# Kernel tuning notes

Measured on AMD Instinct MI355X. Metric: run time of the kernel, lower is better.

Reference implementation:

```python
import jax, jax.numpy as jnp
import numpy as np

B, S, E = 2, 1024, 2048
NH = 8          # num attention heads
KVH = 1         # num key/value heads (GQA)
DH = E // NH    # head dim = 256
CAP = 15.0      # gate soft cap
EPS = 1e-6


def setup_inputs() -> dict:
    key = jax.random.key(0)
    ks = jax.random.split(key, 11)
    g = lambda k, shape, sc=0.02: (jax.random.normal(k, shape, jnp.float32) * sc)
    return {
        "x": jax.random.normal(ks[0], (B, S, E), jnp.float32),
        "Wq": g(ks[1], (E, NH * DH)),
        "Wk": g(ks[2], (E, KVH * DH)),
        "Wv": g(ks[3], (E, KVH * DH)),
        "Wog": g(ks[4], (E, E)),
        "Wi": g(ks[5], (E, NH)),
        "bi": g(ks[6], (NH,), 0.1),
        "Wf": g(ks[7], (E, NH)),
        "bf": jnp.ones((NH,), jnp.float32) * 2.0,  # bias forget gate open, as in xLSTM practice
        "gamma": jnp.ones((E,), jnp.float32),       # multihead layernorm weight
        "Wout": g(ks[8], (E, E)),
    }


def _soft_cap(z):
    return CAP * jnp.tanh(z / CAP)


def _repeat_kv(h, n_rep):
    # (B, KVH, S, DH) -> (B, KVH*n_rep, S, DH)
    if n_rep == 1:
        return h
    b, kvh, s, d = h.shape
    return jnp.broadcast_to(h[:, :, None], (b, kvh, n_rep, s, d)).reshape(b, kvh * n_rep, s, d)


def reference(x, Wq, Wk, Wv, Wog, Wi, bi, Wf, bf, gamma, Wout):
    # --- projections ---
    q = (x @ Wq).reshape(B, S, NH, DH).transpose(0, 2, 1, 3)          # (B,NH,S,DH)
    k = (x @ Wk).reshape(B, S, KVH, DH).transpose(0, 2, 1, 3)         # (B,KVH,S,DH)
    v = (x @ Wv).reshape(B, S, KVH, DH).transpose(0, 2, 1, 3)
    k = _repeat_kv(k, NH // KVH)
    v = _repeat_kv(v, NH // KVH)
    o_preact = x @ Wog                                                # (B,S,E)
    i_pre = _soft_cap(x @ Wi + bi).transpose(0, 2, 1)                 # (B,NH,S)
    f_pre = _soft_cap(x @ Wf + bf).transpose(0, 2, 1)                 # (B,NH,S)

    # --- parallel (stabilized) mLSTM backend ---
    logf = jax.nn.log_sigmoid(f_pre)
    cf = jnp.cumsum(logf, axis=-1)                                    # (B,NH,S)
    mat_logf = cf[:, :, :, None] - cf[:, :, None, :]                  # (B,NH,S,S)
    ltr = jnp.tril(jnp.ones((S, S), dtype=bool))
    mat_logD = jnp.where(ltr, mat_logf, -jnp.inf) + i_pre[:, :, None, :]
    vecM = jnp.max(mat_logD, axis=-1, keepdims=True)                  # (B,NH,S,1)
    matD = jnp.exp(mat_logD - vecM)
    matS = jnp.einsum('bhsd,bhtd->bhst', q, k) * (DH ** -0.5)
    matCt = matS * matD
    vecN = jnp.maximum(jnp.abs(matCt.sum(-1, keepdims=True)), jnp.exp(-vecM))
    matC = matCt / (vecN + EPS)
    h = jnp.einsum('bhst,bhtd->bhsd', matC, v)                        # (B,NH,S,DH)

    # --- multihead layernorm (per-head, float32 reductions) ---
    h = h.transpose(0, 2, 1, 3)                                       # (B,S,NH,DH)
    hf = h.astype(jnp.float32)
    mu = hf.mean(-1, keepdims=True)
    var = hf.var(-1, keepdims=True)
    h_norm = ((hf - mu) * jax.lax.rsqrt(var + EPS)).astype(h.dtype)
    h_norm = (h_norm * gamma.reshape(NH, DH)).reshape(B, S, E)

    # --- output gate + projection ---
    y = (jax.nn.sigmoid(o_preact) * h_norm) @ Wout
    return y
```

## Files before the change

### kernel.cpp

```cpp
#include <hip/hip_runtime.h>
#include <math.h>

#define S_LEN  1024
#define EMB    2048
#define NH_    8
#define DH_    256
#define TOKENS 2048
#define NBH    16
#define NQKVO  4608

typedef __attribute__((ext_vector_type(4))) float    f32x4;
typedef __attribute__((ext_vector_type(8))) _Float16 f16x8;
typedef __attribute__((ext_vector_type(4))) _Float16 f16x4;

__device__ __forceinline__ _Float16 f2h(float f) { return (_Float16)f; }

__device__ __forceinline__ void gload16(const void* g, void* l) {
  __builtin_amdgcn_global_load_lds(
      (const __attribute__((address_space(1))) void*)g,
      (__attribute__((address_space(3))) void*)l, 16, 0, 0);
}

__global__ __launch_bounds__(256) void transpose_all_kernel(
    const float* __restrict__ Wq, const float* __restrict__ Wk,
    const float* __restrict__ Wv, const float* __restrict__ Wog,
    const float* __restrict__ Wout,
    _Float16* __restrict__ WcatT, _Float16* __restrict__ WoutT)
{
  int t = blockIdx.x;
  const float* in; _Float16* out; int ldi, ct;
  if (t < 1024)      { in = Wq;   out = WcatT;                    ldi = 2048; ct = 32; }
  else if (t < 1152) { t -= 1024; in = Wk;  out = WcatT + (long)2048 * EMB; ldi = 256; ct = 4; }
  else if (t < 1280) { t -= 1152; in = Wv;  out = WcatT + (long)2304 * EMB; ldi = 256; ct = 4; }
  else if (t < 2304) { t -= 1280; in = Wog; out = WcatT + (long)2560 * EMB; ldi = 2048; ct = 32; }
  else               { t -= 2304; in = Wout; out = WoutT;         ldi = 2048; ct = 32; }
  const long c0 = (long)(t % ct) * 64, r0 = (long)(t / ct) * 64;
  __shared__ float tl[64][65];
  const int lx = threadIdx.x & 63, ly = threadIdx.x >> 6;
  #pragma unroll
  for (int i = 0; i < 16; ++i)
    tl[ly + i * 4][lx] = in[(r0 + ly + i * 4) * ldi + c0 + lx];
  __syncthreads();
  #pragma unroll
  for (int i = 0; i < 16; ++i)
    out[(c0 + ly + i * 4) * EMB + r0 + lx] = f2h(tl[lx][ly + i * 4]);
}

template<typename TIN>
__global__ __launch_bounds__(256) void transpose_cast_kernel(
    const TIN* __restrict__ in, long ldi, _Float16* __restrict__ out, long ldo,
    long sIn, long sOut)
{
  __shared__ float t[64][65];
  const int lx = threadIdx.x & 63, ly = threadIdx.x >> 6;
  const long r0 = (long)blockIdx.y * 64, c0 = (long)blockIdx.x * 64;
  const TIN* ip = in + (long)blockIdx.z * sIn;
  _Float16* op = out + (long)blockIdx.z * sOut;
  #pragma unroll
  for (int i = 0; i < 16; ++i)
    t[ly + i * 4][lx] = (float)ip[(r0 + ly + i * 4) * ldi + c0 + lx];
  __syncthreads();
  #pragma unroll
  for (int i = 0; i < 16; ++i)
    op[(c0 + ly + i * 4) * ldo + r0 + lx] = f2h(t[lx][ly + i * 4]);
}

template<typename CT, int BM>
__global__ __launch_bounds__(256) void gemm_bt_kernel(
    const _Float16* __restrict__ Ag, const _Float16* __restrict__ Btg,
    CT* __restrict__ Cg, int K, int lda, int ldb, int ldc,
    long sA, long sB, long sC, int zdivB, int mtiles, int causal)
{
  constexpr int MR = BM / 32;
  __shared__ _Float16 As[3][BM * 32];
  __shared__ _Float16 Bs[3][128 * 32];
  const int tid = threadIdx.x;
  const int lane = tid & 63, wid = tid >> 6;
  const int cpx = gridDim.x >> 3;
  const int wg = ((int)blockIdx.x & 7) * cpx + ((int)blockIdx.x >> 3);
  const int m0 = (wg % mtiles) * BM;
  const int n0 = (wg / mtiles) * 128;
  const int z  = blockIdx.z;
  const _Float16* Ap = Ag + (long)z * sA + (long)m0 * lda;
  const _Float16* Bp = Btg + (long)(z / zdivB) * sB + (long)n0 * ldb;
  const int wr = wid >> 1, wc = wid & 1;
  const int lrow = lane & 15, kseg = lane >> 4;
  const int kl = causal ? ((m0 + BM < K) ? m0 + BM : K) : K;

  auto stage = [&](int b, int k0) {
    #pragma unroll
    for (int i = 0; i < BM / 64; ++i) {
      const int cbase = (i * 4 + wid) * 64;
      const int row = (cbase >> 2) + (lane >> 2);
      const int src = ((lane & 3) ^ ((row >> 1) & 3)) * 8;
      gload16(Ap + (long)row * lda + k0 + src, (char*)As[b] + cbase * 16);
    }
    #pragma unroll
    for (int i = 0; i < 2; ++i) {
      const int cbase = (i * 4 + wid) * 64;
      const int row = (cbase >> 2) + (lane >> 2);
      const int src = ((lane & 3) ^ ((row >> 1) & 3)) * 8;
      gload16(Bp + (long)row * ldb + k0 + src, (char*)Bs[b] + cbase * 16);
    }
  };

  const int nt = kl >> 5;
  f32x4 acc[MR][4] = {};
  stage(0, 0);
  if (nt > 1) stage(1, 32);
  for (int t = 0; t < nt; ++t) {
    if (t + 2 < nt) {
      stage((t + 2) % 3, (t + 2) * 32);
      asm volatile("s_waitcnt vmcnt(8)" ::: "memory");
    } else if (t + 1 < nt) {
      asm volatile("s_waitcnt vmcnt(4)" ::: "memory");
    } else {
      asm volatile("s_waitcnt vmcnt(0)" ::: "memory");
    }
    __builtin_amdgcn_s_barrier();
    __builtin_amdgcn_sched_barrier(0);
    const int buf = t % 3;
    f16x8 fa[MR], fb[4];
    #pragma unroll
    for (int m = 0; m < MR; ++m) {
      const int row = wr * (BM / 2) + m * 16 + lrow;
      fa[m] = *(const f16x8*)&As[buf][row * 32 + ((kseg ^ ((row >> 1) & 3)) << 3)];
    }
    #pragma unroll
    for (int n = 0; n < 4; ++n) {
      const int row = wc * 64 + n * 16 + lrow;
      fb[n] = *(const f16x8*)&Bs[buf][row * 32 + ((kseg ^ ((row >> 1) & 3)) << 3)];
    }
    #pragma unroll
    for (int m = 0; m < MR; ++m)
      #pragma unroll
      for (int n = 0; n < 4; ++n)
        acc[m][n] = __builtin_amdgcn_mfma_f32_16x16x32_f16(fa[m], fb[n], acc[m][n], 0, 0, 0);
    __builtin_amdgcn_s_barrier();
  }
  CT* Cp = Cg + (long)z * sC;
  #pragma unroll
  for (int m = 0; m < MR; ++m)
    #pragma unroll
    for (int n = 0; n < 4; ++n)
      #pragma unroll
      for (int i = 0; i < 4; ++i) {
        const int r = m0 + wr * (BM / 2) + m * 16 + kseg * 4 + i;
        const int c = n0 + wc * 64 + n * 16 + lrow;
        Cp[(long)r * ldc + c] = (CT)acc[m][n][i];
      }
}

__global__ __launch_bounds__(256) void proj_if_cast_kernel(
    const float* __restrict__ x, const float* __restrict__ Wi, const float* __restrict__ bi,
    const float* __restrict__ Wf, const float* __restrict__ bfg,
    _Float16* __restrict__ xh, float* __restrict__ ip, float* __restrict__ fp)
{
  const int tok = blockIdx.x;
  const int tid = threadIdx.x;
  const float* xr = x + (long)tok * EMB;
  float ai[8] = {}, af[8] = {};
  #pragma unroll
  for (int j = 0; j < 8; ++j) {
    const int e = tid + j * 256;
    const float xe = xr[e];
    xh[(long)tok * EMB + e] = f2h(xe);
    const float4* wi4 = (const float4*)(Wi + (long)e * 8);
    const float4* wf4 = (const float4*)(Wf + (long)e * 8);
    const float4 a0 = wi4[0], a1 = wi4[1], b0 = wf4[0], b1 = wf4[1];
    ai[0] += xe * a0.x; ai[1] += xe * a0.y; ai[2] += xe * a0.z; ai[3] += xe * a0.w;
    ai[4] += xe * a1.x; ai[5] += xe * a1.y; ai[6] += xe * a1.z; ai[7] += xe * a1.w;
    af[0] += xe * b0.x; af[1] += xe * b0.y; af[2] += xe * b0.z; af[3] += xe * b0.w;
    af[4] += xe * b1.x; af[5] += xe * b1.y; af[6] += xe * b1.z; af[7] += xe * b1.w;
  }
  #pragma unroll
  for (int hh = 0; hh < 8; ++hh)
    for (int off = 32; off; off >>= 1) {
      ai[hh] += __shfl_xor(ai[hh], off);
      af[hh] += __shfl_xor(af[hh], off);
    }
  __shared__ float red[4][16];
  const int lane = tid & 63, wid = tid >> 6;
  if (lane == 0) {
    #pragma unroll
    for (int hh = 0; hh < 8; ++hh) { red[wid][hh] = ai[hh]; red[wid][hh + 8] = af[hh]; }
  }
  __syncthreads();
  if (tid < 16) {
    const float v = red[0][tid] + red[1][tid] + red[2][tid] + red[3][tid];
    const int b = tok >> 10, s = tok & 1023;
    if (tid < 8) {
      const float zv = v + bi[tid];
      ip[(long)(b * NH_ + tid) * S_LEN + s] = 15.0f * tanhf(zv * (1.0f / 15.0f));
    } else {
      const int hh = tid - 8;
      const float zv = v + bfg[hh];
      fp[(long)(b * NH_ + hh) * S_LEN + s] = 15.0f * tanhf(zv * (1.0f / 15.0f));
    }
  }
}

__global__ __launch_bounds__(1024) void gates_kernel(
    const float* __restrict__ fp, const float* __restrict__ ip,
    float* __restrict__ aArr, float* __restrict__ mArr, float* __restrict__ vMArr)
{
  const int bh = blockIdx.x;
  const int s = threadIdx.x;
  __shared__ float sh[1024];
  const float f = fp[(long)bh * S_LEN + s];
  const float lsg = fminf(f, 0.0f) - log1pf(expf(-fabsf(f)));
  float v = lsg;
  sh[s] = v; __syncthreads();
  for (int off = 1; off < 1024; off <<= 1) {
    const float o = (s >= off) ? sh[s - off] : 0.0f;
    __syncthreads();
    v += o; sh[s] = v;
    __syncthreads();
  }
  const float cf = v;
  const float a = ip[(long)bh * S_LEN + s] - cf;
  v = a;
  sh[s] = v; __syncthreads();
  for (int off = 1; off < 1024; off <<= 1) {
    const float o = (s >= off) ? sh[s - off] : -3.0e38f;
    __syncthreads();
    v = fmaxf(v, o); sh[s] = v;
    __syncthreads();
  }
  aArr[(long)bh * S_LEN + s] = a;
  mArr[(long)bh * S_LEN + s] = v;
  vMArr[(long)bh * S_LEN + s] = cf + v;
}

__global__ __launch_bounds__(256) void att_fused_kernel(
    const _Float16* __restrict__ qkvo, const _Float16* __restrict__ vt,
    const float* __restrict__ aArr, const float* __restrict__ mArr,
    const float* __restrict__ vMArr, _Float16* __restrict__ hb)
{
  __shared__ _Float16 Qs[2][32 * 256];
  __shared__ _Float16 Ws[2][32 * 128];
  __shared__ float nsh[2][4][32];
  __shared__ float invs[2][32];
  const int tid = threadIdx.x;
  const int lane = tid & 63, wid = tid >> 6;
  const int bh = blockIdx.y;
  const int b = bh >> 3, h = bh & 7;
  const int r0[2] = { (int)blockIdx.x * 32, (31 - (int)blockIdx.x) * 32 };
  const _Float16* Qg = qkvo + (long)(b * S_LEN) * NQKVO + h * DH_;
  const _Float16* Kg = qkvo + (long)(b * S_LEN) * NQKVO + 2048;
  const _Float16* Vt = vt + (long)b * DH_ * S_LEN;
  const float* aA = aArr + (long)bh * S_LEN;
  const float* mA = mArr + (long)bh * S_LEN;
  const int lrow = lane & 15, kseg = lane >> 4;
  const int tbase = 32 * wid;

  #pragma unroll
  for (int i = 0; i < 8; ++i) {
    const int cbase = (i * 4 + wid) * 64;
    const int c = cbase + lane;
    const int sub = c >> 10, row = (c >> 5) & 31, slot = c & 31;
    gload16(Qg + (long)(r0[sub] + row) * NQKVO + (slot ^ (row & 7)) * 8,
            (char*)Qs + cbase * 16);
  }

  float m_s[2][2][4];
  #pragma unroll
  for (int sub = 0; sub < 2; ++sub)
    #pragma unroll
    for (int m = 0; m < 2; ++m)
      #pragma unroll
      for (int i = 0; i < 4; ++i)
        m_s[sub][m][i] = mA[r0[sub] + m * 16 + kseg * 4 + i];
  __syncthreads();

  f32x4 hacc[2][2][4] = {};
  float nacc[2][2][4] = {};
  for (int n0 = 0; n0 <= r0[1]; n0 += 128) {
    f32x4 acc[2][2][2] = {};
    f16x8 fb[2], fbn[2];
    #pragma unroll
    for (int n = 0; n < 2; ++n)
      fb[n] = *(const f16x8*)(Kg + (long)(n0 + tbase + n * 16 + lrow) * NQKVO + kseg * 8);
    #pragma unroll
    for (int k0 = 0; k0 < DH_; k0 += 32) {
      if (k0 + 32 < DH_) {
        #pragma unroll
        for (int n = 0; n < 2; ++n)
          fbn[n] = *(const f16x8*)(Kg + (long)(n0 + tbase + n * 16 + lrow) * NQKVO + k0 + 32 + kseg * 8);
      }
      const int chunk = (k0 >> 3) + kseg;
      __builtin_amdgcn_s_setprio(1);
      #pragma unroll
      for (int sub = 0; sub < 2; ++sub) {
        if (n0 > r0[sub]) continue;
        #pragma unroll
        for (int m = 0; m < 2; ++m) {
          const int qrow = m * 16 + lrow;
          const f16x8 fa = *(const f16x8*)&Qs[sub][qrow * 256 + ((chunk ^ (qrow & 7)) << 3)];
          #pragma unroll
          for (int n = 0; n < 2; ++n)
            acc[sub][m][n] = __builtin_amdgcn_mfma_f32_16x16x32_f16(fa, fb[n], acc[sub][m][n], 0, 0, 0);
        }
      }
      __builtin_amdgcn_s_setprio(0);
      fb[0] = fbn[0]; fb[1] = fbn[1];
    }
    float a_t[2];
    #pragma unroll
    for (int n = 0; n < 2; ++n) a_t[n] = aA[n0 + tbase + n * 16 + lrow];
    #pragma unroll
    for (int sub = 0; sub < 2; ++sub) {
      if (n0 > r0[sub]) continue;
      #pragma unroll
      for (int m = 0; m < 2; ++m)
        #pragma unroll
        for (int n = 0; n < 2; ++n)
          #pragma unroll
          for (int i = 0; i < 4; ++i) {
            const int sr = m * 16 + kseg * 4 + i;
            const int t  = tbase + n * 16 + lrow;
            float w = 0.0f;
            if (n0 + t <= r0[sub] + sr)
              w = acc[sub][m][n][i] * 0.0625f * expf(a_t[n] - m_s[sub][m][i]);
            nacc[sub][m][i] += w;
            Ws[sub][sr * 128 + (((t >> 3) ^ ((sr & 7) << 1)) << 3) + (t & 7)] = f2h(w);
          }
    }
    f16x8 vb[4], vbn[4];
    #pragma unroll
    for (int n = 0; n < 4; ++n)
      vb[n] = *(const f16x8*)(Vt + (long)(64 * wid + n * 16 + lrow) * S_LEN + n0 + kseg * 8);
    __syncthreads();
    #pragma unroll
    for (int kt = 0; kt < 128; kt += 32) {
      if (kt + 32 < 128) {
        #pragma unroll
        for (int n = 0; n < 4; ++n)
          vbn[n] = *(const f16x8*)(Vt + (long)(64 * wid + n * 16 + lrow) * S_LEN + n0 + kt + 32 + kseg * 8);
      }
      const int chunk = (kt >> 3) + kseg;
      __builtin_amdgcn_s_setprio(1);
      #pragma unroll
      for (int sub = 0; sub < 2; ++sub) {
        if (n0 > r0[sub]) continue;
        #pragma unroll
        for (int m = 0; m < 2; ++m) {
          const int row = m * 16 + lrow;
          const f16x8 wa = *(const f16x8*)&Ws[sub][row * 128 + ((chunk ^ ((row & 7) << 1)) << 3)];
          #pragma unroll
          for (int n = 0; n < 4; ++n)
            hacc[sub][m][n] = __builtin_amdgcn_mfma_f32_16x16x32_f16(wa, vb[n], hacc[sub][m][n], 0, 0, 0);
        }
      }
      __builtin_amdgcn_s_setprio(0);
      #pragma unroll
      for (int n = 0; n < 4; ++n) vb[n] = vbn[n];
    }
    __syncthreads();
  }
  #pragma unroll
  for (int sub = 0; sub < 2; ++sub)
    #pragma unroll
    for (int m = 0; m < 2; ++m)
      #pragma unroll
      for (int i = 0; i < 4; ++i) {
        float v = nacc[sub][m][i];
        v += __shfl_xor(v, 1); v += __shfl_xor(v, 2);
        v += __shfl_xor(v, 4); v += __shfl_xor(v, 8);
        if (lrow == 0) nsh[sub][wid][m * 16 + kseg * 4 + i] = v;
      }
  __syncthreads();
  if (tid < 64) {
    const int sub = tid >> 5, sr = tid & 31;
    const float tot = nsh[sub][0][sr] + nsh[sub][1][sr] + nsh[sub][2][sr] + nsh[sub][3][sr];
    const float vm = vMArr[(long)bh * S_LEN + r0[sub] + sr];
    const float vecN = fmaxf(fabsf(tot), expf(-vm));
    invs[sub][sr] = 1.0f / (vecN + 1e-6f);
  }
  __syncthreads();
  #pragma unroll
  for (int sub = 0; sub < 2; ++sub)
    #pragma unroll
    for (int m = 0; m < 2; ++m)
      #pragma unroll
      for (int n = 0; n < 4; ++n)
        #pragma unroll
        for (int i = 0; i < 4; ++i) {
          const int row = m * 16 + kseg * 4 + i;
          const int d = 64 * wid + n * 16 + lrow;
          hb[((long)bh * S_LEN + r0[sub] + row) * DH_ + d] = f2h(hacc[sub][m][n][i] * invs[sub][row]);
        }
}

__global__ __launch_bounds__(256) void ln_gate_kernel(
    const _Float16* __restrict__ hbuf,
    const _Float16* __restrict__ qkvo, const float* __restrict__ gamma,
    _Float16* __restrict__ u)
{
  const int wid = threadIdx.x >> 6, lane = threadIdx.x & 63;
  const int row = blockIdx.x * 4 + wid;
  const int tok = row >> 3, h = row & 7;
  const int b = tok >> 10, s = tok & 1023;
  const int bh = b * NH_ + h;
  const f16x4 hv = *(const f16x4*)(hbuf + ((long)bh * S_LEN + s) * DH_ + lane * 4);
  const float v0 = (float)hv[0], v1 = (float)hv[1], v2 = (float)hv[2], v3 = (float)hv[3];
  float s1 = v0 + v1 + v2 + v3;
  float s2 = v0 * v0 + v1 * v1 + v2 * v2 + v3 * v3;
  for (int off = 32; off; off >>= 1) { s1 += __shfl_xor(s1, off); s2 += __shfl_xor(s2, off); }
  const float mu = s1 * (1.0f / 256.0f);
  const float var = s2 * (1.0f / 256.0f) - mu * mu;
  const float rs = rsqrtf(var + 1e-6f);
  const float4 g = *(const float4*)(gamma + h * DH_ + lane * 4);
  const f16x4 ov = *(const f16x4*)(qkvo + (long)tok * NQKVO + 2560 + h * DH_ + lane * 4);
  f16x4 res;
  res[0] = f2h((v0 - mu) * rs * g.x * (1.0f / (1.0f + expf(-(float)ov[0]))));
  res[1] = f2h((v1 - mu) * rs * g.y * (1.0f / (1.0f + expf(-(float)ov[1]))));
  res[2] = f2h((v2 - mu) * rs * g.z * (1.0f / (1.0f + expf(-(float)ov[2]))));
  res[3] = f2h((v3 - mu) * rs * g.w * (1.0f / (1.0f + expf(-(float)ov[3]))));
  *(f16x4*)(u + (long)tok * EMB + h * DH_ + lane * 4) = res;
}

extern "C" void kernel_launch(void* const* d_in, const int* in_sizes, int n_in,
                              void* d_out, int out_size, void* d_ws, size_t ws_size,
                              hipStream_t stream)
{
  (void)in_sizes; (void)n_in; (void)out_size; (void)ws_size;
  const float* x     = (const float*)d_in[0];
  const float* Wq    = (const float*)d_in[1];
  const float* Wk    = (const float*)d_in[2];
  const float* Wv    = (const float*)d_in[3];
  const float* Wog   = (const float*)d_in[4];
  const float* Wi    = (const float*)d_in[5];
  const float* bi    = (const float*)d_in[6];
  const float* Wf    = (const float*)d_in[7];
  const float* bfg   = (const float*)d_in[8];
  const float* gamma = (const float*)d_in[9];
  const float* Wout  = (const float*)d_in[10];

  char* base = (char*)d_ws;
  size_t off = 0;
  auto take = [&](size_t bytes) -> char* {
    char* p = base + off;
    off += (bytes + 255) & ~(size_t)255;
    return p;
  };
  _Float16* xh    = (_Float16*)take((size_t)TOKENS * EMB * 2);
  _Float16* WcatT = (_Float16*)take((size_t)NQKVO * EMB * 2);
  _Float16* WoutT = (_Float16*)take((size_t)EMB * EMB * 2);
  _Float16* qkvo  = (_Float16*)take((size_t)TOKENS * NQKVO * 2);
  _Float16* vt    = (_Float16*)take((size_t)2 * DH_ * S_LEN * 2);
  _Float16* hb    = (_Float16*)take((size_t)NBH * S_LEN * DH_ * 2);
  float*    ip    = (float*)take((size_t)NBH * S_LEN * 4);
  float*    fp    = (float*)take((size_t)NBH * S_LEN * 4);
  float*    aA    = (float*)take((size_t)NBH * S_LEN * 4);
  float*    mA    = (float*)take((size_t)NBH * S_LEN * 4);
  float*    vM    = (float*)take((size_t)NBH * S_LEN * 4);
  _Float16* ub    = xh;
  float*    y     = (float*)d_out;

  const dim3 blk(256);
  proj_if_cast_kernel<<<dim3(TOKENS), blk, 0, stream>>>(x, Wi, bi, Wf, bfg, xh, ip, fp);
  transpose_all_kernel<<<dim3(3328), blk, 0, stream>>>(Wq, Wk, Wv, Wog, Wout, WcatT, WoutT);
  gemm_bt_kernel<_Float16, 128><<<dim3(36 * 16), blk, 0, stream>>>(
      xh, WcatT, qkvo, EMB, EMB, EMB, NQKVO, 0L, 0L, 0L, 1, 16, 0);
  transpose_cast_kernel<_Float16><<<dim3(4, 16, 2), blk, 0, stream>>>(
      qkvo + 2304, NQKVO, vt, S_LEN, (long)S_LEN * NQKVO, (long)DH_ * S_LEN);
  gates_kernel<<<dim3(NBH), dim3(1024), 0, stream>>>(fp, ip, aA, mA, vM);
  att_fused_kernel<<<dim3(16, NBH), blk, 0, stream>>>(qkvo, vt, aA, mA, vM, hb);
  ln_gate_kernel<<<dim3(TOKENS * NH_ / 4), blk, 0, stream>>>(hb, qkvo, gamma, ub);
  gemm_bt_kernel<float, 128><<<dim3(16 * 16), blk, 0, stream>>>(
      ub, WoutT, y, EMB, EMB, EMB, EMB, 0L, 0L, 0L, 1, 16, 0);
}
```

Measured before the change: 191.5 us.

## Double attention block to eight waves, splitting key and head-dim work per wave

The fused attention kernel now runs 512 threads (8 waves) per block instead of 256. Each wave handles 16 key columns instead of 32 in the QK^T stage and 32 head-dim columns instead of 64 in the PV stage, and the normalizer reduction now sums over 8 waves. The grid is only 256 blocks, so the aim is more waves in flight to hide latency and lower per-wave register pressure. The cost is more barrier participants and less MFMA work per wave between syncs.

```diff
diff --git a/kernel.cpp b/kernel.cpp
--- a/kernel.cpp
+++ b/kernel.cpp
@@ -232,14 +232,14 @@
   vMArr[(long)bh * S_LEN + s] = cf + v;
 }
 
-__global__ __launch_bounds__(256) void att_fused_kernel(
+__global__ __launch_bounds__(512) void att_fused_kernel(
     const _Float16* __restrict__ qkvo, const _Float16* __restrict__ vt,
     const float* __restrict__ aArr, const float* __restrict__ mArr,
     const float* __restrict__ vMArr, _Float16* __restrict__ hb)
 {
   __shared__ _Float16 Qs[2][32 * 256];
   __shared__ _Float16 Ws[2][32 * 128];
-  __shared__ float nsh[2][4][32];
+  __shared__ float nsh[2][8][32];
   __shared__ float invs[2][32];
   const int tid = threadIdx.x;
   const int lane = tid & 63, wid = tid >> 6;
@@ -252,11 +252,12 @@
   const float* aA = aArr + (long)bh * S_LEN;
   const float* mA = mArr + (long)bh * S_LEN;
   const int lrow = lane & 15, kseg = lane >> 4;
-  const int tbase = 32 * wid;
-
-  #pragma unroll
-  for (int i = 0; i < 8; ++i) {
-    const int cbase = (i * 4 + wid) * 64;
+  const int tbase = 16 * wid;
+  const int dbase = 32 * wid;
+
+  #pragma unroll
+  for (int i = 0; i < 4; ++i) {
+    const int cbase = (i * 8 + wid) * 64;
     const int c = cbase + lane;
     const int sub = c >> 10, row = (c >> 5) & 31, slot = c & 31;
     gload16(Qg + (long)(r0[sub] + row) * NQKVO + (slot ^ (row & 7)) * 8,
@@ -273,21 +274,16 @@
         m_s[sub][m][i] = mA[r0[sub] + m * 16 + kseg * 4 + i];
   __syncthreads();
 
-  f32x4 hacc[2][2][4] = {};
+  f32x4 hacc[2][2][2] = {};
   float nacc[2][2][4] = {};
   for (int n0 = 0; n0 <= r0[1]; n0 += 128) {
-    f32x4 acc[2][2][2] = {};
-    f16x8 fb[2], fbn[2];
-    #pragma unroll
-    for (int n = 0; n < 2; ++n)
-      fb[n] = *(const f16x8*)(Kg + (long)(n0 + tbase + n * 16 + lrow) * NQKVO + kseg * 8);
+    f32x4 acc[2][2] = {};
+    f16x8 fb, fbn;
+    fb = *(const f16x8*)(Kg + (long)(n0 + tbase + lrow) * NQKVO + kseg * 8);
     #pragma unroll
     for (int k0 = 0; k0 < DH_; k0 += 32) {
-      if (k0 + 32 < DH_) {
-        #pragma unroll
-        for (int n = 0; n < 2; ++n)
-          fbn[n] = *(const f16x8*)(Kg + (long)(n0 + tbase + n * 16 + lrow) * NQKVO + k0 + 32 + kseg * 8);
-      }
+      if (k0 + 32 < DH_)
+        fbn = *(const f16x8*)(Kg + (long)(n0 + tbase + lrow) * NQKVO + k0 + 32 + kseg * 8);
       const int chunk = (k0 >> 3) + kseg;
       __builtin_amdgcn_s_setprio(1);
       #pragma unroll
@@ -297,46 +293,40 @@
         for (int m = 0; m < 2; ++m) {
           const int qrow = m * 16 + lrow;
           const f16x8 fa = *(const f16x8*)&Qs[sub][qrow * 256 + ((chunk ^ (qrow & 7)) << 3)];
-          #pragma unroll
-          for (int n = 0; n < 2; ++n)
-            acc[sub][m][n] = __builtin_amdgcn_mfma_f32_16x16x32_f16(fa, fb[n], acc[sub][m][n], 0, 0, 0);
+          acc[sub][m] = __builtin_amdgcn_mfma_f32_16x16x32_f16(fa, fb, acc[sub][m], 0, 0, 0);
         }
       }
       __builtin_amdgcn_s_setprio(0);
-      fb[0] = fbn[0]; fb[1] = fbn[1];
-    }
-    float a_t[2];
-    #pragma unroll
-    for (int n = 0; n < 2; ++n) a_t[n] = aA[n0 + tbase + n * 16 + lrow];
+      fb = fbn;
+    }
+    const float a_t = aA[n0 + tbase + lrow];
     #pragma unroll
     for (int sub = 0; sub < 2; ++sub) {
       if (n0 > r0[sub]) continue;
       #pragma unroll
       for (int m = 0; m < 2; ++m)
         #pragma unroll
-        for (int n = 0; n < 2; ++n)
-          #pragma unroll
-          for (int i = 0; i < 4; ++i) {
-            const int sr = m * 16 + kseg * 4 + i;
-            const int t  = tbase + n * 16 + lrow;
-            float w = 0.0f;
-            if (n0 + t <= r0[sub] + sr)
-              w = acc[sub][m][n][i] * 0.0625f * expf(a_t[n] - m_s[sub][m][i]);
-            nacc[sub][m][i] += w;
-            Ws[sub][sr * 128 + (((t >> 3) ^ ((sr & 7) << 1)) << 3) + (t & 7)] = f2h(w);
-          }
-    }
-    f16x8 vb[4], vbn[4];
-    #pragma unroll
-    for (int n = 0; n < 4; ++n)
-      vb[n] = *(const f16x8*)(Vt + (long)(64 * wid + n * 16 + lrow) * S_LEN + n0 + kseg * 8);
+        for (int i = 0; i < 4; ++i) {
+          const int sr = m * 16 + kseg * 4 + i;
+          const int t  = tbase + lrow;
+          float w = 0.0f;
+          if (n0 + t <= r0[sub] + sr)
+            w = acc[sub][m][i] * 0.0625f * expf(a_t - m_s[sub][m][i]);
+          nacc[sub][m][i] += w;
+          Ws[sub][sr * 128 + (((t >> 3) ^ ((sr & 7) << 1)) << 3) + (t & 7)] = f2h(w);
+        }
+    }
+    f16x8 vb[2], vbn[2];
+    #pragma unroll
+    for (int n = 0; n < 2; ++n)
+      vb[n] = *(const f16x8*)(Vt + (long)(dbase + n * 16 + lrow) * S_LEN + n0 + kseg * 8);
     __syncthreads();
     #pragma unroll
     for (int kt = 0; kt < 128; kt += 32) {
       if (kt + 32 < 128) {
         #pragma unroll
-        for (int n = 0; n < 4; ++n)
-          vbn[n] = *(const f16x8*)(Vt + (long)(64 * wid + n * 16 + lrow) * S_LEN + n0 + kt + 32 + kseg * 8);
+        for (int n = 0; n < 2; ++n)
+          vbn[n] = *(const f16x8*)(Vt + (long)(dbase + n * 16 + lrow) * S_LEN + n0 + kt + 32 + kseg * 8);
       }
       const int chunk = (kt >> 3) + kseg;
       __builtin_amdgcn_s_setprio(1);
@@ -348,13 +338,12 @@
           const int row = m * 16 + lrow;
           const f16x8 wa = *(const f16x8*)&Ws[sub][row * 128 + ((chunk ^ ((row & 7) << 1)) << 3)];
           #pragma unroll
-          for (int n = 0; n < 4; ++n)
+          for (int n = 0; n < 2; ++n)
             hacc[sub][m][n] = __builtin_amdgcn_mfma_f32_16x16x32_f16(wa, vb[n], hacc[sub][m][n], 0, 0, 0);
         }
       }
       __builtin_amdgcn_s_setprio(0);
-      #pragma unroll
-      for (int n = 0; n < 4; ++n) vb[n] = vbn[n];
+      vb[0] = vbn[0]; vb[1] = vbn[1];
     }
     __syncthreads();
   }
@@ -372,7 +361,9 @@
   __syncthreads();
   if (tid < 64) {
     const int sub = tid >> 5, sr = tid & 31;
-    const float tot = nsh[sub][0][sr] + nsh[sub][1][sr] + nsh[sub][2][sr] + nsh[sub][3][sr];
+    float tot = 0.0f;
+    #pragma unroll
+    for (int w = 0; w < 8; ++w) tot += nsh[sub][w][sr];
     const float vm = vMArr[(long)bh * S_LEN + r0[sub] + sr];
     const float vecN = fmaxf(fabsf(tot), expf(-vm));
     invs[sub][sr] = 1.0f / (vecN + 1e-6f);
@@ -383,11 +374,11 @@
     #pragma unroll
     for (int m = 0; m < 2; ++m)
       #pragma unroll
-      for (int n = 0; n < 4; ++n)
+      for (int n = 0; n < 2; ++n)
         #pragma unroll
         for (int i = 0; i < 4; ++i) {
           const int row = m * 16 + kseg * 4 + i;
-          const int d = 64 * wid + n * 16 + lrow;
+          const int d = dbase + n * 16 + lrow;
           hb[((long)bh * S_LEN + r0[sub] + row) * DH_ + d] = f2h(hacc[sub][m][n][i] * invs[sub][row]);
         }
 }
@@ -466,7 +457,7 @@
   transpose_cast_kernel<_Float16><<<dim3(4, 16, 2), blk, 0, stream>>>(
       qkvo + 2304, NQKVO, vt, S_LEN, (long)S_LEN * NQKVO, (long)DH_ * S_LEN);
   gates_kernel<<<dim3(NBH), dim3(1024), 0, stream>>>(fp, ip, aA, mA, vM);
-  att_fused_kernel<<<dim3(16, NBH), blk, 0, stream>>>(qkvo, vt, aA, mA, vM, hb);
+  att_fused_kernel<<<dim3(16, NBH), dim3(512), 0, stream>>>(qkvo, vt, aA, mA, vM, hb);
   ln_gate_kernel<<<dim3(TOKENS * NH_ / 4), blk, 0, stream>>>(hb, qkvo, gamma, ub);
   gemm_bt_kernel<float, 128><<<dim3(16 * 16), blk, 0, stream>>>(
       ub, WoutT, y, EMB, EMB, EMB, EMB, 0L, 0L, 0L, 1, 16, 0);
```

Result: faster. 187.3 us (-2.2%).
